# Performance work log

Measured on AMD Instinct MI355X. Metric: run time of the kernel, lower is better.

Reference implementation:

```python
import jax, jax.numpy as jnp
import numpy as np

N_NODES = 8192
N_EDGES = 262144
N_VIEWS = 2


def setup_inputs() -> dict:
    key = jax.random.key(0)
    k1, k2, k3, k4, k5, k6 = jax.random.split(key, 6)
    x = jax.random.normal(k1, (N_NODES, 512), dtype=jnp.float32)
    # Glorot-ish scaling for GCN weights
    W1 = jax.random.normal(k2, (512, 256), dtype=jnp.float32) * (1.0 / np.sqrt(512))
    W2 = jax.random.normal(k3, (256, 128), dtype=jnp.float32) * (1.0 / np.sqrt(256))
    edge_vals = jax.random.uniform(k4, (N_EDGES,), dtype=jnp.float32)
    edge_rows = jax.random.randint(k5, (N_EDGES,), 0, N_NODES, dtype=jnp.int32)
    edge_cols = jax.random.randint(k6, (N_EDGES,), 0, N_NODES, dtype=jnp.int32)
    return {"x": x, "W1": W1, "W2": W2, "edge_vals": edge_vals,
            "edge_rows": edge_rows, "edge_cols": edge_cols}


def reference(x, W1, W2, edge_vals, edge_rows, edge_cols):
    # GraphConvolution: support = x @ W ; out = spmm(adj, support) ; act (relu, dropout=0)
    def spmm(h):
        # out[i] = sum_e A[rows[e], cols[e]] * h[cols[e]]  -- irregular gather + segment reduce
        return jax.ops.segment_sum(edge_vals[:, None] * h[edge_cols], edge_rows,
                                   num_segments=N_NODES)

    # Forward quirk in the source: every view uses adjs[0], and mean over n_views
    # identical embeddings == a single pass, so one spmm per layer is exact.
    h = jax.nn.relu(spmm(x @ W1))        # [N, 256]
    z = jax.nn.relu(spmm(h @ W2))        # [N, 128]  (self.embeddings)

    # InnerProductDecoder with act = identity (lambda x: x from Model_2 default)
    rec = z @ z.T                         # [N, N]
    rec_views = jnp.stack([rec] * N_VIEWS, axis=0)  # n_views identical decoders
    return z, rec_views
```

## Files before the change

kernel.cpp:

```cpp
#include <hip/hip_runtime.h>

#define NN 8192
#define NE 262144

typedef short bf16x8 __attribute__((ext_vector_type(8)));
typedef float f32x16 __attribute__((ext_vector_type(16)));
typedef float f32x4 __attribute__((ext_vector_type(4)));

__device__ __forceinline__ unsigned short f2bf(float f) {
  unsigned u = __float_as_uint(f);
  u += 0x7fffu + ((u >> 16) & 1u);
  return (unsigned short)(u >> 16);
}
__device__ __forceinline__ float bflo(unsigned u) { return __uint_as_float(u << 16); }
__device__ __forceinline__ float bfhi(unsigned u) { return __uint_as_float(u & 0xffff0000u); }

__global__ void k_prep(const float* __restrict__ x, const float* __restrict__ W1,
                       const float* __restrict__ W2, unsigned short* __restrict__ xb,
                       unsigned short* __restrict__ W1t, unsigned short* __restrict__ W2t,
                       int* __restrict__ counts) {
  int id = blockIdx.x * blockDim.x + threadIdx.x;
  int stride = gridDim.x * blockDim.x;
  for (int t = id; t < (NN * 512) / 4; t += stride) {
    float4 v = *(const float4*)(x + (size_t)t * 4);
    unsigned lo = (unsigned)f2bf(v.x) | ((unsigned)f2bf(v.y) << 16);
    unsigned hi = (unsigned)f2bf(v.z) | ((unsigned)f2bf(v.w) << 16);
    *(uint2*)(xb + (size_t)t * 4) = make_uint2(lo, hi);
  }
  for (int t = id; t < 512 * 256; t += stride) {
    int k = t >> 8, c = t & 255;
    W1t[c * 512 + k] = f2bf(W1[t]);
  }
  for (int t = id; t < 256 * 128; t += stride) {
    int k = t >> 7, c = t & 127;
    W2t[c * 256 + k] = f2bf(W2[t]);
  }
  for (int t = id; t < NN; t += stride) counts[t] = 0;
}

__global__ void k_hist(const int* __restrict__ rows, int* __restrict__ counts) {
  int id = blockIdx.x * blockDim.x + threadIdx.x;
  if (id < NE) atomicAdd(&counts[rows[id]], 1);
}

__global__ void k_scan(const int* __restrict__ counts, int* __restrict__ starts,
                       int* __restrict__ cursor) {
  __shared__ int sums[1024];
  int t = threadIdx.x;
  int base = t * 8;
  int local[8];
  int s = 0;
  #pragma unroll
  for (int i = 0; i < 8; ++i) { local[i] = s; s += counts[base + i]; }
  sums[t] = s;
  __syncthreads();
  for (int off = 1; off < 1024; off <<= 1) {
    int v = 0;
    if (t >= off) v = sums[t - off];
    __syncthreads();
    sums[t] += v;
    __syncthreads();
  }
  int pre = sums[t] - s;
  #pragma unroll
  for (int i = 0; i < 8; ++i) {
    starts[base + i] = pre + local[i];
    cursor[base + i] = pre + local[i];
  }
  if (t == 1023) starts[NN] = sums[1023];
}

__global__ void k_scatter(const int* __restrict__ rows, const float* __restrict__ vals,
                          const int* __restrict__ cols, int* __restrict__ cursor,
                          float* __restrict__ ev_s, int* __restrict__ ec_s) {
  int id = blockIdx.x * blockDim.x + threadIdx.x;
  if (id < NE) {
    int pos = atomicAdd(&cursor[rows[id]], 1);
    ev_s[pos] = vals[id];
    ec_s[pos] = cols[id];
  }
}

template <int K, int N>
__global__ __launch_bounds__(512) void k_gemm(const unsigned short* __restrict__ Ab,
                                              const unsigned short* __restrict__ Bt,
                                              unsigned short* __restrict__ Cb) {
  __shared__ unsigned char As[128 * 64 * 2];
  __shared__ unsigned char Bs[64 * 64 * 2];
  const int tid = threadIdx.x;
  const int r0 = blockIdx.x * 128, c0 = blockIdx.y * 64;
  const int wid = tid >> 6, lane = tid & 63;
  const int wr = wid >> 1, wc = wid & 1;
  const int lr = lane & 31, lg = lane >> 5;

  f32x16 acc = {};

  for (int kc = 0; kc < K; kc += 64) {
    __syncthreads();
    #pragma unroll
    for (int q = tid; q < 1024; q += 512) {
      int r = q >> 3, s = q & 7;
      float4 v = *(const float4*)(Ab + (size_t)(r0 + r) * K + kc + s * 8);
      *(float4*)(As + r * 128 + ((s * 16) ^ ((r & 7) << 4))) = v;
    }
    {
      int q = tid;
      if (q < 512) {
        int r = q >> 3, s = q & 7;
        float4 v = *(const float4*)(Bt + (size_t)(c0 + r) * K + kc + s * 8);
        *(float4*)(Bs + r * 128 + ((s * 16) ^ ((r & 7) << 4))) = v;
      }
    }
    __syncthreads();
    #pragma unroll
    for (int ks = 0; ks < 4; ++ks) {
      int brow = wc * 32 + lr;
      bf16x8 bf = *(const bf16x8*)(Bs + brow * 128 + ((ks * 32 + lg * 16) ^ ((brow & 7) << 4)));
      int arow = wr * 32 + lr;
      bf16x8 af = *(const bf16x8*)(As + arow * 128 + ((ks * 32 + lg * 16) ^ ((arow & 7) << 4)));
      acc = __builtin_amdgcn_mfma_f32_32x32x16_bf16(bf, af, acc, 0, 0, 0);
    }
  }
  {
    int row = r0 + wr * 32 + lr;
    #pragma unroll
    for (int g = 0; g < 4; ++g) {
      unsigned lo = (unsigned)f2bf(acc[4 * g + 0]) | ((unsigned)f2bf(acc[4 * g + 1]) << 16);
      unsigned hi = (unsigned)f2bf(acc[4 * g + 2]) | ((unsigned)f2bf(acc[4 * g + 3]) << 16);
      int colc = c0 + wc * 32 + 8 * g + 4 * lg;
      *(uint2*)(Cb + (size_t)row * N + colc) = make_uint2(lo, hi);
    }
  }
}

template <int F>
__global__ __launch_bounds__(256) void k_spmm(const int* __restrict__ starts,
                                              const float* __restrict__ ev_s,
                                              const int* __restrict__ ec_s,
                                              const unsigned short* __restrict__ Sb,
                                              float* __restrict__ outF,
                                              unsigned short* __restrict__ outB) {
  constexpr int V = F / 64;
  int gw = (blockIdx.x * blockDim.x + threadIdx.x) >> 6;
  int lane = threadIdx.x & 63;
  if (gw >= NN) return;
  int s = starts[gw], e = starts[gw + 1];
  float acc[V];
  #pragma unroll
  for (int v = 0; v < V; ++v) acc[v] = 0.f;
  for (int j = s; j < e; ++j) {
    float w = ev_s[j];
    int c = ec_s[j];
    if constexpr (V == 4) {
      uint2 t = *(const uint2*)(Sb + (size_t)c * F + lane * 4);
      acc[0] += w * bflo(t.x); acc[1] += w * bfhi(t.x);
      acc[2] += w * bflo(t.y); acc[3] += w * bfhi(t.y);
    } else {
      unsigned t = *(const unsigned*)(Sb + (size_t)c * F + lane * 2);
      acc[0] += w * bflo(t); acc[1] += w * bfhi(t);
    }
  }
  #pragma unroll
  for (int v = 0; v < V; ++v) acc[v] = fmaxf(acc[v], 0.f);
  if constexpr (V == 4) {
    unsigned lo = (unsigned)f2bf(acc[0]) | ((unsigned)f2bf(acc[1]) << 16);
    unsigned hi = (unsigned)f2bf(acc[2]) | ((unsigned)f2bf(acc[3]) << 16);
    *(uint2*)(outB + (size_t)gw * F + lane * 4) = make_uint2(lo, hi);
  } else {
    unsigned lo = (unsigned)f2bf(acc[0]) | ((unsigned)f2bf(acc[1]) << 16);
    *(unsigned int*)(outB + (size_t)gw * F + lane * 2) = lo;
    if (outF) {
      *(float2*)(outF + (size_t)gw * F + lane * 2) = make_float2(acc[0], acc[1]);
    }
  }
}

__global__ __launch_bounds__(256) void k_rec(const unsigned short* __restrict__ zb,
                                             float* __restrict__ out0,
                                             float* __restrict__ out1) {
  __shared__ unsigned char lds[49152];
  unsigned char* Ai = lds;
  unsigned char* Bj = lds + 16384;
  const int tid = threadIdx.x;
  const int i0 = blockIdx.y * 64, j0 = blockIdx.x * 128;

  for (int q = tid; q < 1024; q += 256) {
    int r = q >> 4, s = q & 15;
    float4 v = *(const float4*)(zb + (size_t)(i0 + r) * 128 + s * 8);
    *(float4*)(Ai + r * 256 + ((s * 16) ^ ((r & 15) << 4))) = v;
  }
  for (int q = tid; q < 2048; q += 256) {
    int r = q >> 4, s = q & 15;
    float4 v = *(const float4*)(zb + (size_t)(j0 + r) * 128 + s * 8);
    *(float4*)(Bj + r * 256 + ((s * 16) ^ ((r & 15) << 4))) = v;
  }
  __syncthreads();

  const int wid = tid >> 6, lane = tid & 63;
  const int wrow = wid >> 1, wcol = wid & 1;
  const int lr = lane & 31, lg = lane >> 5;

  f32x16 acc[2] = {};
  #pragma unroll
  for (int ks = 0; ks < 8; ++ks) {
    int arow = wrow * 32 + lr;
    bf16x8 af = *(const bf16x8*)(Ai + arow * 256 + ((ks * 32 + lg * 16) ^ ((arow & 15) << 4)));
    #pragma unroll
    for (int m = 0; m < 2; ++m) {
      int brow = wcol * 64 + m * 32 + lr;
      bf16x8 bf = *(const bf16x8*)(Bj + brow * 256 + ((ks * 32 + lg * 16) ^ ((brow & 15) << 4)));
      acc[m] = __builtin_amdgcn_mfma_f32_32x32x16_bf16(bf, af, acc[m], 0, 0, 0);
    }
  }

  __syncthreads();
  float* T = (float*)lds;
  {
    int row = wrow * 32 + lr;
    #pragma unroll
    for (int m = 0; m < 2; ++m) {
      #pragma unroll
      for (int q = 0; q < 4; ++q) {
        int col = wcol * 64 + m * 32 + 8 * q + 4 * lg;
        f32x4 v = {acc[m][4 * q + 0], acc[m][4 * q + 1], acc[m][4 * q + 2], acc[m][4 * q + 3]};
        *(f32x4*)(T + row * 132 + col) = v;
      }
    }
  }
  __syncthreads();
  {
    int rr = tid >> 5, cc = (tid & 31) * 4;
    #pragma unroll
    for (int p = 0; p < 8; ++p) {
      int row = p * 8 + rr;
      f32x4 v = *(const f32x4*)(T + row * 132 + cc);
      size_t idx = (size_t)(i0 + row) * NN + (size_t)(j0 + cc);
      *(f32x4*)(out0 + idx) = v;
      *(f32x4*)(out1 + idx) = v;
    }
  }
}

extern "C" void kernel_launch(void* const* d_in, const int* in_sizes, int n_in,
                              void* d_out, int out_size, void* d_ws, size_t ws_size,
                              hipStream_t stream) {
  const float* x     = (const float*)d_in[0];
  const float* W1    = (const float*)d_in[1];
  const float* W2    = (const float*)d_in[2];
  const float* evals = (const float*)d_in[3];
  const int*   erows = (const int*)d_in[4];
  const int*   ecols = (const int*)d_in[5];

  float* out_z   = (float*)d_out;
  float* out_r0  = out_z + (size_t)NN * 128;
  float* out_r1  = out_r0 + (size_t)NN * NN;

  char* w = (char*)d_ws;
  unsigned short* W1t = (unsigned short*)w;  w += 256 * 512 * 2;
  unsigned short* W2t = (unsigned short*)w;  w += 128 * 256 * 2;
  unsigned short* xb  = (unsigned short*)w;  w += (size_t)NN * 512 * 2;
  unsigned short* g1  = (unsigned short*)w;  w += (size_t)NN * 256 * 2;
  unsigned short* h1  = (unsigned short*)w;  w += (size_t)NN * 256 * 2;
  unsigned short* g2  = (unsigned short*)w;  w += (size_t)NN * 128 * 2;
  unsigned short* zb  = (unsigned short*)w;  w += (size_t)NN * 128 * 2;
  int*   counts = (int*)w;                   w += NN * 4;
  int*   starts = (int*)w;                   w += (NN + 8) * 4;
  int*   cursor = (int*)w;                   w += NN * 4;
  float* ev_s   = (float*)w;                 w += NE * 4;
  int*   ec_s   = (int*)w;                   w += NE * 4;

  k_prep<<<256, 256, 0, stream>>>(x, W1, W2, xb, W1t, W2t, counts);
  k_hist<<<NE / 256, 256, 0, stream>>>(erows, counts);
  k_scan<<<1, 1024, 0, stream>>>(counts, starts, cursor);
  k_scatter<<<NE / 256, 256, 0, stream>>>(erows, evals, ecols, cursor, ev_s, ec_s);

  k_gemm<512, 256><<<dim3(64, 4), 512, 0, stream>>>(xb, W1t, g1);
  k_spmm<256><<<NN / 4, 256, 0, stream>>>(starts, ev_s, ec_s, g1, nullptr, h1);
  k_gemm<256, 128><<<dim3(64, 2), 512, 0, stream>>>(h1, W2t, g2);
  k_spmm<128><<<NN / 4, 256, 0, stream>>>(starts, ev_s, ec_s, g2, out_z, zb);
  k_rec<<<dim3(64, 128), 256, 0, stream>>>(zb, out_r0, out_r1);
}
```

Baseline: 653.2 us.

## Fuse x bf16 conversion into GEMM, pack edge pairs, shrink rec tile

The first GEMM now reads fp32 x directly and converts it to bf16 while staging into LDS, so the separate conversion pass and its 8 MB bf16 round trip are gone. Edge values and column indices are packed into one int2 array so each SpMM step does a single 8-byte load. The z·zᵀ output kernel uses 64x64 tiles instead of 64x128, giving twice as many blocks with less LDS each. The costs are extra conversion work in the GEMM's load path and more redundant reads of z in the output kernel.

After: 655.7 us. About the same (+0.4%).

```diff
diff --git a/kernel.cpp b/kernel.cpp
--- a/kernel.cpp
+++ b/kernel.cpp
@@ -15,18 +15,11 @@
 __device__ __forceinline__ float bflo(unsigned u) { return __uint_as_float(u << 16); }
 __device__ __forceinline__ float bfhi(unsigned u) { return __uint_as_float(u & 0xffff0000u); }
 
-__global__ void k_prep(const float* __restrict__ x, const float* __restrict__ W1,
-                       const float* __restrict__ W2, unsigned short* __restrict__ xb,
+__global__ void k_prep(const float* __restrict__ W1, const float* __restrict__ W2,
                        unsigned short* __restrict__ W1t, unsigned short* __restrict__ W2t,
                        int* __restrict__ counts) {
   int id = blockIdx.x * blockDim.x + threadIdx.x;
   int stride = gridDim.x * blockDim.x;
-  for (int t = id; t < (NN * 512) / 4; t += stride) {
-    float4 v = *(const float4*)(x + (size_t)t * 4);
-    unsigned lo = (unsigned)f2bf(v.x) | ((unsigned)f2bf(v.y) << 16);
-    unsigned hi = (unsigned)f2bf(v.z) | ((unsigned)f2bf(v.w) << 16);
-    *(uint2*)(xb + (size_t)t * 4) = make_uint2(lo, hi);
-  }
   for (int t = id; t < 512 * 256; t += stride) {
     int k = t >> 8, c = t & 255;
     W1t[c * 512 + k] = f2bf(W1[t]);
@@ -72,17 +65,17 @@
 
 __global__ void k_scatter(const int* __restrict__ rows, const float* __restrict__ vals,
                           const int* __restrict__ cols, int* __restrict__ cursor,
-                          float* __restrict__ ev_s, int* __restrict__ ec_s) {
+                          int2* __restrict__ ep) {
   int id = blockIdx.x * blockDim.x + threadIdx.x;
   if (id < NE) {
     int pos = atomicAdd(&cursor[rows[id]], 1);
-    ev_s[pos] = vals[id];
-    ec_s[pos] = cols[id];
-  }
-}
-
-template <int K, int N>
-__global__ __launch_bounds__(512) void k_gemm(const unsigned short* __restrict__ Ab,
+    ep[pos] = make_int2(__float_as_int(vals[id]), cols[id]);
+  }
+}
+
+template <int K, int N, bool AF32>
+__global__ __launch_bounds__(512) void k_gemm(const float* __restrict__ Af,
+                                              const unsigned short* __restrict__ Ab,
                                               const unsigned short* __restrict__ Bt,
                                               unsigned short* __restrict__ Cb) {
   __shared__ unsigned char As[128 * 64 * 2];
@@ -100,16 +93,24 @@
     #pragma unroll
     for (int q = tid; q < 1024; q += 512) {
       int r = q >> 3, s = q & 7;
-      float4 v = *(const float4*)(Ab + (size_t)(r0 + r) * K + kc + s * 8);
-      *(float4*)(As + r * 128 + ((s * 16) ^ ((r & 7) << 4))) = v;
-    }
-    {
-      int q = tid;
-      if (q < 512) {
-        int r = q >> 3, s = q & 7;
-        float4 v = *(const float4*)(Bt + (size_t)(c0 + r) * K + kc + s * 8);
-        *(float4*)(Bs + r * 128 + ((s * 16) ^ ((r & 7) << 4))) = v;
+      if constexpr (AF32) {
+        const float* gp = Af + (size_t)(r0 + r) * K + kc + s * 8;
+        float4 v0 = *(const float4*)gp;
+        float4 v1 = *(const float4*)(gp + 4);
+        unsigned a = (unsigned)f2bf(v0.x) | ((unsigned)f2bf(v0.y) << 16);
+        unsigned b = (unsigned)f2bf(v0.z) | ((unsigned)f2bf(v0.w) << 16);
+        unsigned c = (unsigned)f2bf(v1.x) | ((unsigned)f2bf(v1.y) << 16);
+        unsigned d = (unsigned)f2bf(v1.z) | ((unsigned)f2bf(v1.w) << 16);
+        *(uint4*)(As + r * 128 + ((s * 16) ^ ((r & 7) << 4))) = make_uint4(a, b, c, d);
+      } else {
+        float4 v = *(const float4*)(Ab + (size_t)(r0 + r) * K + kc + s * 8);
+        *(float4*)(As + r * 128 + ((s * 16) ^ ((r & 7) << 4))) = v;
       }
+    }
+    if (tid < 512) {
+      int r = tid >> 3, s = tid & 7;
+      float4 v = *(const float4*)(Bt + (size_t)(c0 + r) * K + kc + s * 8);
+      *(float4*)(Bs + r * 128 + ((s * 16) ^ ((r & 7) << 4))) = v;
     }
     __syncthreads();
     #pragma unroll
@@ -135,8 +136,7 @@
 
 template <int F>
 __global__ __launch_bounds__(256) void k_spmm(const int* __restrict__ starts,
-                                              const float* __restrict__ ev_s,
-                                              const int* __restrict__ ec_s,
+                                              const int2* __restrict__ ep,
                                               const unsigned short* __restrict__ Sb,
                                               float* __restrict__ outF,
                                               unsigned short* __restrict__ outB) {
@@ -149,8 +149,9 @@
   #pragma unroll
   for (int v = 0; v < V; ++v) acc[v] = 0.f;
   for (int j = s; j < e; ++j) {
-    float w = ev_s[j];
-    int c = ec_s[j];
+    int2 ed = ep[j];
+    float w = __int_as_float(ed.x);
+    int c = ed.y;
     if constexpr (V == 4) {
       uint2 t = *(const uint2*)(Sb + (size_t)c * F + lane * 4);
       acc[0] += w * bflo(t.x); acc[1] += w * bfhi(t.x);
@@ -178,18 +179,18 @@
 __global__ __launch_bounds__(256) void k_rec(const unsigned short* __restrict__ zb,
                                              float* __restrict__ out0,
                                              float* __restrict__ out1) {
-  __shared__ unsigned char lds[49152];
+  __shared__ unsigned char lds[32768];
   unsigned char* Ai = lds;
   unsigned char* Bj = lds + 16384;
   const int tid = threadIdx.x;
-  const int i0 = blockIdx.y * 64, j0 = blockIdx.x * 128;
+  const int i0 = blockIdx.y * 64, j0 = blockIdx.x * 64;
 
   for (int q = tid; q < 1024; q += 256) {
     int r = q >> 4, s = q & 15;
     float4 v = *(const float4*)(zb + (size_t)(i0 + r) * 128 + s * 8);
     *(float4*)(Ai + r * 256 + ((s * 16) ^ ((r & 15) << 4))) = v;
   }
-  for (int q = tid; q < 2048; q += 256) {
+  for (int q = tid; q < 1024; q += 256) {
     int r = q >> 4, s = q & 15;
     float4 v = *(const float4*)(zb + (size_t)(j0 + r) * 128 + s * 8);
     *(float4*)(Bj + r * 256 + ((s * 16) ^ ((r & 15) << 4))) = v;
@@ -197,43 +198,37 @@
   __syncthreads();
 
   const int wid = tid >> 6, lane = tid & 63;
-  const int wrow = wid >> 1, wcol = wid & 1;
+  const int wr = wid >> 1, wc = wid & 1;
   const int lr = lane & 31, lg = lane >> 5;
 
-  f32x16 acc[2] = {};
+  f32x16 acc = {};
   #pragma unroll
   for (int ks = 0; ks < 8; ++ks) {
-    int arow = wrow * 32 + lr;
+    int arow = wr * 32 + lr;
     bf16x8 af = *(const bf16x8*)(Ai + arow * 256 + ((ks * 32 + lg * 16) ^ ((arow & 15) << 4)));
-    #pragma unroll
-    for (int m = 0; m < 2; ++m) {
-      int brow = wcol * 64 + m * 32 + lr;
-      bf16x8 bf = *(const bf16x8*)(Bj + brow * 256 + ((ks * 32 + lg * 16) ^ ((brow & 15) << 4)));
-      acc[m] = __builtin_amdgcn_mfma_f32_32x32x16_bf16(bf, af, acc[m], 0, 0, 0);
-    }
+    int brow = wc * 32 + lr;
+    bf16x8 bf = *(const bf16x8*)(Bj + brow * 256 + ((ks * 32 + lg * 16) ^ ((brow & 15) << 4)));
+    acc = __builtin_amdgcn_mfma_f32_32x32x16_bf16(bf, af, acc, 0, 0, 0);
   }
 
   __syncthreads();
   float* T = (float*)lds;
   {
-    int row = wrow * 32 + lr;
-    #pragma unroll
-    for (int m = 0; m < 2; ++m) {
-      #pragma unroll
-      for (int q = 0; q < 4; ++q) {
-        int col = wcol * 64 + m * 32 + 8 * q + 4 * lg;
-        f32x4 v = {acc[m][4 * q + 0], acc[m][4 * q + 1], acc[m][4 * q + 2], acc[m][4 * q + 3]};
-        *(f32x4*)(T + row * 132 + col) = v;
-      }
+    int row = wr * 32 + lr;
+    #pragma unroll
+    for (int q = 0; q < 4; ++q) {
+      int col = wc * 32 + 8 * q + 4 * lg;
+      f32x4 v = {acc[4 * q + 0], acc[4 * q + 1], acc[4 * q + 2], acc[4 * q + 3]};
+      *(f32x4*)(T + row * 68 + col) = v;
     }
   }
   __syncthreads();
   {
-    int rr = tid >> 5, cc = (tid & 31) * 4;
-    #pragma unroll
-    for (int p = 0; p < 8; ++p) {
-      int row = p * 8 + rr;
-      f32x4 v = *(const f32x4*)(T + row * 132 + cc);
+    int rr = tid >> 4, cc = (tid & 15) * 4;
+    #pragma unroll
+    for (int p = 0; p < 4; ++p) {
+      int row = p * 16 + rr;
+      f32x4 v = *(const f32x4*)(T + row * 68 + cc);
       size_t idx = (size_t)(i0 + row) * NN + (size_t)(j0 + cc);
       *(f32x4*)(out0 + idx) = v;
       *(f32x4*)(out1 + idx) = v;
@@ -258,7 +253,6 @@
   char* w = (char*)d_ws;
   unsigned short* W1t = (unsigned short*)w;  w += 256 * 512 * 2;
   unsigned short* W2t = (unsigned short*)w;  w += 128 * 256 * 2;
-  unsigned short* xb  = (unsigned short*)w;  w += (size_t)NN * 512 * 2;
   unsigned short* g1  = (unsigned short*)w;  w += (size_t)NN * 256 * 2;
   unsigned short* h1  = (unsigned short*)w;  w += (size_t)NN * 256 * 2;
   unsigned short* g2  = (unsigned short*)w;  w += (size_t)NN * 128 * 2;
@@ -266,17 +260,16 @@
   int*   counts = (int*)w;                   w += NN * 4;
   int*   starts = (int*)w;                   w += (NN + 8) * 4;
   int*   cursor = (int*)w;                   w += NN * 4;
-  float* ev_s   = (float*)w;                 w += NE * 4;
-  int*   ec_s   = (int*)w;                   w += NE * 4;
-
-  k_prep<<<256, 256, 0, stream>>>(x, W1, W2, xb, W1t, W2t, counts);
+  int2*  ep     = (int2*)w;                  w += (size_t)NE * 8;
+
+  k_prep<<<256, 256, 0, stream>>>(W1, W2, W1t, W2t, counts);
   k_hist<<<NE / 256, 256, 0, stream>>>(erows, counts);
   k_scan<<<1, 1024, 0, stream>>>(counts, starts, cursor);
-  k_scatter<<<NE / 256, 256, 0, stream>>>(erows, evals, ecols, cursor, ev_s, ec_s);
-
-  k_gemm<512, 256><<<dim3(64, 4), 512, 0, stream>>>(xb, W1t, g1);
-  k_spmm<256><<<NN / 4, 256, 0, stream>>>(starts, ev_s, ec_s, g1, nullptr, h1);
-  k_gemm<256, 128><<<dim3(64, 2), 512, 0, stream>>>(h1, W2t, g2);
-  k_spmm<128><<<NN / 4, 256, 0, stream>>>(starts, ev_s, ec_s, g2, out_z, zb);
-  k_rec<<<dim3(64, 128), 256, 0, stream>>>(zb, out_r0, out_r1);
-}
+  k_scatter<<<NE / 256, 256, 0, stream>>>(erows, evals, ecols, cursor, ep);
+
+  k_gemm<512, 256, true><<<dim3(64, 4), 512, 0, stream>>>(x, nullptr, W1t, g1);
+  k_spmm<256><<<NN / 4, 256, 0, stream>>>(starts, ep, g1, nullptr, h1);
+  k_gemm<256, 128, false><<<dim3(64, 2), 512, 0, stream>>>(nullptr, h1, W2t, g2);
+  k_spmm<128><<<NN / 4, 256, 0, stream>>>(starts, ep, g2, out_z, zb);
+  k_rec<<<dim3(128, 128), 256, 0, stream>>>(zb, out_r0, out_r1);
+}
```
